# Performance work log

Measured on AMD Instinct MI355X. Metric: run time of the kernel, lower is better.

## Reference

```python
import jax, jax.numpy as jnp
import numpy as np

K_NODES = 4096
SEQ_L = 32
D_MODEL = 128
D_FF = 512
N_EDGES = 65536
LN_EPS = 1e-5
NEG_SLOPE = 0.2  # PyG GATConv default leaky_relu slope


def setup_inputs() -> dict:
    key = jax.random.key(0)
    ks = jax.random.split(key, 12)
    s = 0.02
    D, F = D_MODEL, D_FF
    return {
        "x": jax.random.normal(ks[0], (1, K_NODES, SEQ_L, D), jnp.float32),
        "edge_index": jax.random.randint(ks[1], (1, 2, N_EDGES), 0, K_NODES, dtype=jnp.int64),
        # temporal TransformerEncoderLayer params (norm_first, 1 head, gelu)
        "ln1_g": jnp.ones((D,), jnp.float32), "ln1_b": jnp.zeros((D,), jnp.float32),
        "qkv_w": jax.random.normal(ks[2], (3 * D, D), jnp.float32) * s,
        "qkv_b": jnp.zeros((3 * D,), jnp.float32),
        "out_w": jax.random.normal(ks[3], (D, D), jnp.float32) * s,
        "out_b": jnp.zeros((D,), jnp.float32),
        "ln2_g": jnp.ones((D,), jnp.float32), "ln2_b": jnp.zeros((D,), jnp.float32),
        "ff1_w": jax.random.normal(ks[4], (F, D), jnp.float32) * s,
        "ff1_b": jnp.zeros((F,), jnp.float32),
        "ff2_w": jax.random.normal(ks[5], (D, F), jnp.float32) * s,
        "ff2_b": jnp.zeros((D,), jnp.float32),
        # GATConv params (heads=1, concat -> out dim D)
        "gat_w": jax.random.normal(ks[6], (D, D), jnp.float32) * s,
        "att_src": jax.random.normal(ks[7], (D,), jnp.float32) * s,
        "att_dst": jax.random.normal(ks[8], (D,), jnp.float32) * s,
        "gat_b": jnp.zeros((D,), jnp.float32),
    }


def _ln(x, g, b):
    m = x.mean(-1, keepdims=True)
    v = ((x - m) ** 2).mean(-1, keepdims=True)
    return (x - m) * jax.lax.rsqrt(v + LN_EPS) * g + b


def _temporal(x, ln1_g, ln1_b, qkv_w, qkv_b, out_w, out_b, ln2_g, ln2_b,
              ff1_w, ff1_b, ff2_w, ff2_b):
    # x: [N, L, D]; pre-norm single-head self-attention + GELU FFN
    D = x.shape[-1]
    h = _ln(x, ln1_g, ln1_b)
    qkv = h @ qkv_w.T + qkv_b
    q, k, v = jnp.split(qkv, 3, axis=-1)
    scores = jnp.einsum('nqd,nkd->nqk', q, k) / jnp.sqrt(jnp.asarray(D, x.dtype))
    a = jax.nn.softmax(scores, axis=-1)
    attn = jnp.einsum('nqk,nkd->nqd', a, v) @ out_w.T + out_b
    x = x + attn
    h = _ln(x, ln2_g, ln2_b)
    ff = jax.nn.gelu(h @ ff1_w.T + ff1_b, approximate=False) @ ff2_w.T + ff2_b
    return x + ff


def _gat(x0, src, dst, gat_w, att_src, att_dst, gat_b):
    # x0: [K, L, D]; vectorized over L (replaces the per-timestep python loop)
    K = x0.shape[0]
    h = jnp.einsum('kld,ed->kle', x0, gat_w)              # [K, L, D]
    a_s = jnp.einsum('kld,d->kl', h, att_src)             # [K, L]
    a_d = jnp.einsum('kld,d->kl', h, att_dst)
    e = jax.nn.leaky_relu(a_s[src] + a_d[dst], NEG_SLOPE)  # [E', L]
    m = jax.ops.segment_max(e, dst, num_segments=K)
    ex = jnp.exp(e - m[dst])
    denom = jax.ops.segment_sum(ex, dst, num_segments=K)
    alpha = ex / (denom[dst] + 1e-16)
    out = jax.ops.segment_sum(h[src] * alpha[..., None], dst, num_segments=K)
    return out + gat_b


def reference(x, edge_index, ln1_g, ln1_b, qkv_w, qkv_b, out_w, out_b,
              ln2_g, ln2_b, ff1_w, ff1_b, ff2_w, ff2_b,
              gat_w, att_src, att_dst, gat_b):
    B, K, L, D = x.shape
    xt = _temporal(x.reshape(B * K, L, D), ln1_g, ln1_b, qkv_w, qkv_b,
                   out_w, out_b, ln2_g, ln2_b, ff1_w, ff1_b, ff2_w, ff2_b)
    xt = xt.reshape(B, K, L, D)
    # GATConv adds self-loops by default
    loops = jnp.arange(K, dtype=edge_index.dtype)
    src = jnp.concatenate([edge_index[0, 0], loops])
    dst = jnp.concatenate([edge_index[0, 1], loops])
    out0 = _gat(xt[0], src, dst, gat_w, att_src, att_dst, gat_b)  # [K, L, D]
    res = jnp.zeros_like(x).at[0].set(out0)
    return res
```

## Files before the change

kernel.cpp:

```cpp
#include <hip/hip_runtime.h>

#define KNODES 4096
#define SEQL 32
#define DM 128
#define DFF 512
#define NEDGE 65536
#define NETOT (NEDGE + KNODES)

typedef float f32x4 __attribute__((ext_vector_type(4)));
typedef short s16x8 __attribute__((ext_vector_type(8)));
typedef short s16x4 __attribute__((ext_vector_type(4)));

#define MFMA16(a, b, c) __builtin_amdgcn_mfma_f32_16x16x32_bf16(a, b, c, 0, 0, 0)

#define F_OUT 96
#define F_FF1 128
#define F_FF2 256
#define F_GAT 384
#define NFRAG 416

__device__ __forceinline__ short f2bf(float f) {
  union { float f; unsigned u; } v; v.f = f;
  unsigned r = (v.u + 0x7FFFu + ((v.u >> 16) & 1u)) >> 16;
  return (short)r;
}

__device__ __forceinline__ float gelu_exact(float v) {
  return 0.5f * v * (1.f + erff(v * 0.70710678118654752440f));
}

__device__ __forceinline__ void ln_to_bf16(const float* XF, short* AB,
                                           const float* __restrict__ g,
                                           const float* __restrict__ b,
                                           int r, int cb) {
  const float* xr = XF + r * 132 + cb;
  float v[8]; float s = 0.f, ss = 0.f;
#pragma unroll
  for (int i = 0; i < 8; ++i) { v[i] = xr[i]; s += v[i]; ss += v[i] * v[i]; }
  s += __shfl_xor(s, 1); ss += __shfl_xor(ss, 1);
  s += __shfl_xor(s, 2); ss += __shfl_xor(ss, 2);
  s += __shfl_xor(s, 4); ss += __shfl_xor(ss, 4);
  s += __shfl_xor(s, 8); ss += __shfl_xor(ss, 8);
  const float mean = s * (1.f / 128.f);
  const float var = ss * (1.f / 128.f) - mean * mean;
  const float rs = rsqrtf(var + 1e-5f);
  const float* gp = g + cb; const float* bp = b + cb;
  short o[8];
#pragma unroll
  for (int i = 0; i < 8; ++i) o[i] = f2bf((v[i] - mean) * rs * gp[i] + bp[i]);
  *(s16x8*)(AB + r * 136 + cb) = *(s16x8*)o;
}

__global__ __launch_bounds__(512, 4) void temporal_kernel(
    const float* __restrict__ x,
    const float* __restrict__ ln1_g, const float* __restrict__ ln1_b,
    const short* __restrict__ wpk, const float* __restrict__ qkv_b,
    const float* __restrict__ out_b,
    const float* __restrict__ ln2_g, const float* __restrict__ ln2_b,
    const float* __restrict__ ff1_b, const float* __restrict__ ff2_b,
    const float* __restrict__ att_src, const float* __restrict__ att_dst,
    short* __restrict__ h_out, float* __restrict__ as_out, float* __restrict__ ad_out) {
  __shared__ __align__(16) char smem[53248];
  float* XF = (float*)smem;
  short* AB = (short*)(smem + 16896);
  float* Sf = (float*)(smem + 16896);
  short* Pb = (short*)(smem + 21504);
  short* Qb = (short*)(smem + 25600);
  short* Kb = (short*)(smem + 34304);
  short* Fb = (short*)(smem + 25600);
  short* Vt = (short*)(smem + 43008);

  const int t = threadIdx.x;
  const int w = t >> 6;
  const int lane = t & 63;
  const int q = lane >> 4, c = lane & 15;
  const int n = blockIdx.x;
  const int r16 = t >> 4, cb8 = (t & 15) * 8;

#define WPK(f) ((const s16x8*)(wpk + (size_t)(f) * 512 + lane * 8))

  s16x8 bwq[3][4];
#pragma unroll
  for (int ii = 0; ii < 3; ++ii)
#pragma unroll
    for (int kt = 0; kt < 4; ++kt)
      bwq[ii][kt] = *WPK((w * 3 + ii) * 4 + kt);

  {
#pragma unroll
    for (int i = t; i < 1024; i += 512) {
      const int row = i >> 5, c4i = i & 31;
      *(float4*)(XF + row * 132 + c4i * 4) =
          *(const float4*)(x + (size_t)n * (SEQL * DM) + i * 4);
    }
  }
  __syncthreads();

  ln_to_bf16(XF, AB, ln1_g, ln1_b, r16, cb8);
  __syncthreads();

  {
    s16x8 a[2][4];
#pragma unroll
    for (int mt = 0; mt < 2; ++mt)
#pragma unroll
      for (int kt = 0; kt < 4; ++kt)
        a[mt][kt] = *(const s16x8*)(AB + (mt * 16 + c) * 136 + kt * 32 + q * 8);
#pragma unroll
    for (int ii = 0; ii < 3; ++ii) {
      const int n0 = (w * 3 + ii) * 16;
      f32x4 acc0 = {0.f, 0.f, 0.f, 0.f}, acc1 = {0.f, 0.f, 0.f, 0.f};
#pragma unroll
      for (int kt = 0; kt < 4; ++kt) {
        acc0 = MFMA16(a[0][kt], bwq[ii][kt], acc0);
        acc1 = MFMA16(a[1][kt], bwq[ii][kt], acc1);
      }
      const float bias = qkv_b[n0 + c];
      if (n0 < 128) {
#pragma unroll
        for (int i = 0; i < 4; ++i) {
          Qb[(q * 4 + i) * 136 + n0 + c] = f2bf(acc0[i] + bias);
          Qb[(16 + q * 4 + i) * 136 + n0 + c] = f2bf(acc1[i] + bias);
        }
      } else if (n0 < 256) {
        const int cc = n0 - 128 + c;
#pragma unroll
        for (int i = 0; i < 4; ++i) {
          Kb[(q * 4 + i) * 136 + cc] = f2bf(acc0[i] + bias);
          Kb[(16 + q * 4 + i) * 136 + cc] = f2bf(acc1[i] + bias);
        }
      } else {
        const int d = n0 - 256 + c;
        s16x4 p0, p1;
#pragma unroll
        for (int i = 0; i < 4; ++i) { p0[i] = f2bf(acc0[i] + bias); p1[i] = f2bf(acc1[i] + bias); }
        *(s16x4*)(Vt + d * 40 + q * 4) = p0;
        *(s16x4*)(Vt + d * 40 + 16 + q * 4) = p1;
      }
    }
  }
  __syncthreads();

  if (w < 4) {
    const int mt = w & 1, nt = w >> 1;
    s16x8 aq[4], bk[4];
#pragma unroll
    for (int kt = 0; kt < 4; ++kt) {
      aq[kt] = *(const s16x8*)(Qb + (mt * 16 + c) * 136 + kt * 32 + q * 8);
      bk[kt] = *(const s16x8*)(Kb + (nt * 16 + c) * 136 + kt * 32 + q * 8);
    }
    f32x4 acc = {0.f, 0.f, 0.f, 0.f};
#pragma unroll
    for (int kt = 0; kt < 4; ++kt) acc = MFMA16(aq[kt], bk[kt], acc);
#pragma unroll
    for (int i = 0; i < 4; ++i)
      Sf[(mt * 16 + q * 4 + i) * 36 + nt * 16 + c] = acc[i] * 0.08838834764831845f;
  }
  __syncthreads();

  if (t < 256) {
    const int r8 = t >> 3, c4 = (t & 7) * 4;
    float4 sv = *(const float4*)(Sf + r8 * 36 + c4);
    float mx = fmaxf(fmaxf(sv.x, sv.y), fmaxf(sv.z, sv.w));
    mx = fmaxf(mx, __shfl_xor(mx, 1));
    mx = fmaxf(mx, __shfl_xor(mx, 2));
    mx = fmaxf(mx, __shfl_xor(mx, 4));
    float e0 = expf(sv.x - mx), e1 = expf(sv.y - mx), e2 = expf(sv.z - mx), e3 = expf(sv.w - mx);
    float sum = e0 + e1 + e2 + e3;
    sum += __shfl_xor(sum, 1);
    sum += __shfl_xor(sum, 2);
    sum += __shfl_xor(sum, 4);
    const float inv = 1.f / sum;
    s16x4 pw; pw[0] = f2bf(e0 * inv); pw[1] = f2bf(e1 * inv); pw[2] = f2bf(e2 * inv); pw[3] = f2bf(e3 * inv);
    *(s16x4*)(Pb + r8 * 40 + c4) = pw;
  }
  __syncthreads();

  s16x8 bwp[4];
  {
#pragma unroll
    for (int kt = 0; kt < 4; ++kt) bwp[kt] = *WPK(F_OUT + w * 4 + kt);
    s16x8 ap0 = *(const s16x8*)(Pb + c * 40 + q * 8);
    s16x8 ap1 = *(const s16x8*)(Pb + (16 + c) * 40 + q * 8);
    const int d0 = w * 16;
    s16x8 bv = *(const s16x8*)(Vt + (d0 + c) * 40 + q * 8);
    f32x4 acc0 = {0.f, 0.f, 0.f, 0.f}, acc1 = {0.f, 0.f, 0.f, 0.f};
    acc0 = MFMA16(ap0, bv, acc0);
    acc1 = MFMA16(ap1, bv, acc1);
#pragma unroll
    for (int i = 0; i < 4; ++i) {
      Qb[(q * 4 + i) * 136 + d0 + c] = f2bf(acc0[i]);
      Qb[(16 + q * 4 + i) * 136 + d0 + c] = f2bf(acc1[i]);
    }
  }
  __syncthreads();

  {
    s16x8 aa[2][4];
#pragma unroll
    for (int mt = 0; mt < 2; ++mt)
#pragma unroll
      for (int kt = 0; kt < 4; ++kt)
        aa[mt][kt] = *(const s16x8*)(Qb + (mt * 16 + c) * 136 + kt * 32 + q * 8);
    const int n0 = w * 16;
    f32x4 acc0 = {0.f, 0.f, 0.f, 0.f}, acc1 = {0.f, 0.f, 0.f, 0.f};
#pragma unroll
    for (int kt = 0; kt < 4; ++kt) {
      acc0 = MFMA16(aa[0][kt], bwp[kt], acc0);
      acc1 = MFMA16(aa[1][kt], bwp[kt], acc1);
    }
    const float bias = out_b[n0 + c];
#pragma unroll
    for (int i = 0; i < 4; ++i) {
      XF[(q * 4 + i) * 132 + n0 + c] += acc0[i] + bias;
      XF[(16 + q * 4 + i) * 132 + n0 + c] += acc1[i] + bias;
    }
  }
  __syncthreads();

  ln_to_bf16(XF, AB, ln2_g, ln2_b, r16, cb8);
  __syncthreads();

  {
    s16x8 af[2][4];
#pragma unroll
    for (int mt = 0; mt < 2; ++mt)
#pragma unroll
      for (int kt = 0; kt < 4; ++kt)
        af[mt][kt] = *(const s16x8*)(AB + (mt * 16 + c) * 136 + kt * 32 + q * 8);
    f32x4 facc0 = {0.f, 0.f, 0.f, 0.f}, facc1 = {0.f, 0.f, 0.f, 0.f};

    for (int ch = 0; ch < 2; ++ch) {
      s16x8 bw1[2][4], bw2[8];
#pragma unroll
      for (int ii = 0; ii < 2; ++ii)
#pragma unroll
        for (int kt = 0; kt < 4; ++kt)
          bw1[ii][kt] = *WPK(F_FF1 + (ch * 16 + w * 2 + ii) * 4 + kt);
#pragma unroll
      for (int kt = 0; kt < 8; ++kt)
        bw2[kt] = *WPK(F_FF2 + w * 16 + ch * 8 + kt);

#pragma unroll
      for (int ii = 0; ii < 2; ++ii) {
        const int ntl = w * 2 + ii;
        const int n0g = ch * 256 + ntl * 16;
        f32x4 acc0 = {0.f, 0.f, 0.f, 0.f}, acc1 = {0.f, 0.f, 0.f, 0.f};
#pragma unroll
        for (int kt = 0; kt < 4; ++kt) {
          acc0 = MFMA16(af[0][kt], bw1[ii][kt], acc0);
          acc1 = MFMA16(af[1][kt], bw1[ii][kt], acc1);
        }
        const float bias = ff1_b[n0g + c];
#pragma unroll
        for (int i = 0; i < 4; ++i) {
          Fb[(q * 4 + i) * 264 + ntl * 16 + c] = f2bf(gelu_exact(acc0[i] + bias));
          Fb[(16 + q * 4 + i) * 264 + ntl * 16 + c] = f2bf(gelu_exact(acc1[i] + bias));
        }
      }
      __syncthreads();
#pragma unroll
      for (int kt = 0; kt < 8; ++kt) {
        s16x8 a0 = *(const s16x8*)(Fb + c * 264 + kt * 32 + q * 8);
        s16x8 a1 = *(const s16x8*)(Fb + (16 + c) * 264 + kt * 32 + q * 8);
        facc0 = MFMA16(a0, bw2[kt], facc0);
        facc1 = MFMA16(a1, bw2[kt], facc1);
      }
      __syncthreads();
    }
    {
      const int n0 = w * 16;
      const float bias = ff2_b[n0 + c];
#pragma unroll
      for (int i = 0; i < 4; ++i) {
        const int r0 = q * 4 + i, r1 = 16 + q * 4 + i;
        AB[r0 * 136 + n0 + c] = f2bf(XF[r0 * 132 + n0 + c] + facc0[i] + bias);
        AB[r1 * 136 + n0 + c] = f2bf(XF[r1 * 132 + n0 + c] + facc1[i] + bias);
      }
    }
  }
  s16x8 bwg[4];
#pragma unroll
  for (int kt = 0; kt < 4; ++kt) bwg[kt] = *WPK(F_GAT + w * 4 + kt);
  __syncthreads();

  {
    s16x8 ag[2][4];
#pragma unroll
    for (int mt = 0; mt < 2; ++mt)
#pragma unroll
      for (int kt = 0; kt < 4; ++kt)
        ag[mt][kt] = *(const s16x8*)(AB + (mt * 16 + c) * 136 + kt * 32 + q * 8);
    const int n0 = w * 16;
    f32x4 acc0 = {0.f, 0.f, 0.f, 0.f}, acc1 = {0.f, 0.f, 0.f, 0.f};
#pragma unroll
    for (int kt = 0; kt < 4; ++kt) {
      acc0 = MFMA16(ag[0][kt], bwg[kt], acc0);
      acc1 = MFMA16(ag[1][kt], bwg[kt], acc1);
    }
#pragma unroll
    for (int i = 0; i < 4; ++i) {
      const int r0 = q * 4 + i, r1 = 16 + q * 4 + i;
      XF[r0 * 132 + n0 + c] = acc0[i];
      XF[r1 * 132 + n0 + c] = acc1[i];
    }
  }
  __syncthreads();

  {
    const int row = t >> 4;
    const float* xr = XF + row * 132 + cb8;
    short o[8];
#pragma unroll
    for (int i = 0; i < 8; ++i) o[i] = f2bf(xr[i]);
    *(s16x8*)(h_out + ((size_t)row * KNODES + n) * DM + cb8) = *(s16x8*)o;
  }

  if (t < 64) {
    const int row = t & 31;
    const float* vec = (t < 32) ? att_src : att_dst;
    const float* hr = XF + row * 132;
    float s = 0.f;
#pragma unroll
    for (int d = 0; d < DM; d += 4)
      s += hr[d] * vec[d] + hr[d + 1] * vec[d + 1] + hr[d + 2] * vec[d + 2] + hr[d + 3] * vec[d + 3];
    if (t < 32) as_out[n * SEQL + row] = s;
    else        ad_out[n * SEQL + row] = s;
  }
}

__global__ void cvt_weights(const float* __restrict__ qkv_w, const float* __restrict__ out_w,
                            const float* __restrict__ ff1_w, const float* __restrict__ ff2_w,
                            const float* __restrict__ gat_w, short* __restrict__ wpk) {
  const int u = blockIdx.x * 256 + threadIdx.x;
  if (u >= NFRAG * 64) return;
  const int f = u >> 6, lane = u & 63;
  const int q = lane >> 4, c = lane & 15;
  const float* src; int row, kt, ld;
  if (f < F_OUT)       { src = qkv_w; ld = 128; int g = f;         row = (g >> 2) * 16 + c; kt = g & 3; }
  else if (f < F_FF1)  { src = out_w; ld = 128; int g = f - F_OUT; row = (g >> 2) * 16 + c; kt = g & 3; }
  else if (f < F_FF2)  { src = ff1_w; ld = 128; int g = f - F_FF1; row = (g >> 2) * 16 + c; kt = g & 3; }
  else if (f < F_GAT)  { src = ff2_w; ld = 512; int g = f - F_FF2; row = (g >> 4) * 16 + c; kt = g & 15; }
  else                 { src = gat_w; ld = 128; int g = f - F_GAT; row = (g >> 2) * 16 + c; kt = g & 3; }
  const float* p = src + row * ld + kt * 32 + q * 8;
  const float4 v0 = *(const float4*)p;
  const float4 v1 = *(const float4*)(p + 4);
  s16x8 o;
  o[0] = f2bf(v0.x); o[1] = f2bf(v0.y); o[2] = f2bf(v0.z); o[3] = f2bf(v0.w);
  o[4] = f2bf(v1.x); o[5] = f2bf(v1.y); o[6] = f2bf(v1.z); o[7] = f2bf(v1.w);
  *(s16x8*)(wpk + (size_t)f * 512 + lane * 8) = o;
}

__global__ void zero_counts(int* counts) {
  int i = blockIdx.x * 256 + threadIdx.x;
  if (i < KNODES) counts[i] = 0;
}

__global__ void hist_kernel(const int* __restrict__ ei, int* counts) {
  int i = blockIdx.x * 256 + threadIdx.x;
  if (i < NETOT) {
    int dst = (i < NEDGE) ? ei[NEDGE + i] : (i - NEDGE);
    atomicAdd(&counts[dst], 1);
  }
}

__global__ void scan_kernel(const int* __restrict__ counts, int* offs, int* cursor) {
  __shared__ int tmp[1024];
  const int t = threadIdx.x;
  const int base = t * 4;
  int c0 = counts[base], c1 = counts[base + 1], c2 = counts[base + 2], c3 = counts[base + 3];
  const int s = c0 + c1 + c2 + c3;
  tmp[t] = s;
  __syncthreads();
  for (int off = 1; off < 1024; off <<= 1) {
    int v = (t >= off) ? tmp[t - off] : 0;
    __syncthreads();
    tmp[t] += v;
    __syncthreads();
  }
  int o = tmp[t] - s;
  offs[base] = o; cursor[base] = o; o += c0;
  offs[base + 1] = o; cursor[base + 1] = o; o += c1;
  offs[base + 2] = o; cursor[base + 2] = o; o += c2;
  offs[base + 3] = o; cursor[base + 3] = o; o += c3;
  if (t == 1023) offs[KNODES] = o;
}

__global__ void scatter_kernel(const int* __restrict__ ei, int* cursor, int* __restrict__ csr) {
  int i = blockIdx.x * 256 + threadIdx.x;
  if (i < NETOT) {
    int src, dst;
    if (i < NEDGE) { src = ei[i]; dst = ei[NEDGE + i]; }
    else           { src = dst = i - NEDGE; }
    int pos = atomicAdd(&cursor[dst], 1);
    csr[pos] = src;
  }
}

#define ECH 16
__global__ __launch_bounds__(64) void gat_aggregate(
    const short* __restrict__ h, const float* __restrict__ as_g, const float* __restrict__ ad_g,
    const int* __restrict__ offs, const int* __restrict__ csr,
    const float* __restrict__ gat_b, float* __restrict__ out) {
  __shared__ float ew[ECH * 5];
  __shared__ int   srcs[ECH];

  const int t = threadIdx.x;
  const int lg = blockIdx.x;
  const int n = blockIdx.y;
  const int l0 = lg * 4;

  const int s = t >> 2, lr = t & 3;
  const int r = t >> 4, cl = (t & 15) * 8;

  const float adv = ad_g[n * SEQL + l0 + lr];
  const int beg = offs[n], end = offs[n + 1];
  const size_t rbase = ((size_t)(l0 + r) * KNODES) * DM + cl;

  float dpart = 0.f;
  float acc[8];
#pragma unroll
  for (int j = 0; j < 8; ++j) acc[j] = 0.f;

  for (int cb = beg; cb < end; cb += ECH) {
    const int cnt = min(ECH, end - cb);
    if (s < cnt) {
      const int src = csr[cb + s];
      if (lr == 0) srcs[s] = src;
      float v = as_g[src * SEQL + l0 + lr] + adv;
      v = v > 0.f ? v : 0.2f * v;
      const float e = __expf(v);
      ew[s * 5 + lr] = e;
      dpart += e;
    }
    __syncthreads();

    s16x8 p0, p1, p2, p3;
#define GLOAD(dst, idx)                                                        \
    if ((idx) < cnt)                                                           \
      dst = *(const s16x8*)(h + rbase + (size_t)srcs[idx] * DM)
    GLOAD(p0, 0); GLOAD(p1, 1); GLOAD(p2, 2); GLOAD(p3, 3);

#define CONSUME(p, idx)                                                        \
    if ((idx) < cnt) {                                                         \
      const float wgt = ew[(idx) * 5 + r];                                     \
      const unsigned* pu = (const unsigned*)&(p);                              \
      _Pragma("unroll")                                                        \
      for (int j = 0; j < 4; ++j) {                                           \
        acc[2 * j]     += wgt * __uint_as_float(pu[j] << 16);                  \
        acc[2 * j + 1] += wgt * __uint_as_float(pu[j] & 0xFFFF0000u);          \
      }                                                                        \
    }

    for (int ss = 0; ss < cnt; ss += 4) {
      s16x8 n0, n1, n2, n3;
      GLOAD(n0, ss + 4); GLOAD(n1, ss + 5); GLOAD(n2, ss + 6); GLOAD(n3, ss + 7);
      CONSUME(p0, ss);
      CONSUME(p1, ss + 1);
      CONSUME(p2, ss + 2);
      CONSUME(p3, ss + 3);
      p0 = n0; p1 = n1; p2 = n2; p3 = n3;
    }
#undef GLOAD
#undef CONSUME
    __syncthreads();
  }

  dpart += __shfl_xor(dpart, 4);
  dpart += __shfl_xor(dpart, 8);
  dpart += __shfl_xor(dpart, 16);
  dpart += __shfl_xor(dpart, 32);
  const float iv = 1.f / (__shfl(dpart, r) + 1e-16f);

  const float4 b0 = *(const float4*)(gat_b + cl);
  const float4 b1 = *(const float4*)(gat_b + cl + 4);
  f32x4 o0, o1;
  o0[0] = acc[0] * iv + b0.x; o0[1] = acc[1] * iv + b0.y;
  o0[2] = acc[2] * iv + b0.z; o0[3] = acc[3] * iv + b0.w;
  o1[0] = acc[4] * iv + b1.x; o1[1] = acc[5] * iv + b1.y;
  o1[2] = acc[6] * iv + b1.z; o1[3] = acc[7] * iv + b1.w;
  float* op = out + (size_t)n * (SEQL * DM) + (l0 + r) * DM + cl;
  __builtin_nontemporal_store(o0, (f32x4*)op);
  __builtin_nontemporal_store(o1, (f32x4*)(op + 4));
}

extern "C" void kernel_launch(void* const* d_in, const int* in_sizes, int n_in,
                              void* d_out, int out_size, void* d_ws, size_t ws_size,
                              hipStream_t stream) {
  const float* x       = (const float*)d_in[0];
  const int* ei        = (const int*)d_in[1];
  const float* ln1_g   = (const float*)d_in[2];
  const float* ln1_b   = (const float*)d_in[3];
  const float* qkv_w   = (const float*)d_in[4];
  const float* qkv_b   = (const float*)d_in[5];
  const float* out_w   = (const float*)d_in[6];
  const float* out_b   = (const float*)d_in[7];
  const float* ln2_g   = (const float*)d_in[8];
  const float* ln2_b   = (const float*)d_in[9];
  const float* ff1_w   = (const float*)d_in[10];
  const float* ff1_b   = (const float*)d_in[11];
  const float* ff2_w   = (const float*)d_in[12];
  const float* ff2_b   = (const float*)d_in[13];
  const float* gat_w   = (const float*)d_in[14];
  const float* att_src = (const float*)d_in[15];
  const float* att_dst = (const float*)d_in[16];
  const float* gat_b   = (const float*)d_in[17];
  float* out = (float*)d_out;

  short* h    = (short*)d_ws;
  float* as_g = (float*)(h + (size_t)KNODES * SEQL * DM);
  float* ad_g = as_g + KNODES * SEQL;
  int* counts = (int*)(ad_g + KNODES * SEQL);
  int* offs   = counts + KNODES;
  int* cursor = offs + KNODES + 1;
  int* csr    = cursor + KNODES;
  size_t wofs = (size_t)((char*)(csr + NETOT) - (char*)d_ws);
  wofs = (wofs + 1023) & ~(size_t)1023;
  short* wpk = (short*)((char*)d_ws + wofs);

  cvt_weights<<<(NFRAG * 64 + 255) / 256, 256, 0, stream>>>(qkv_w, out_w, ff1_w, ff2_w, gat_w, wpk);
  zero_counts<<<(KNODES + 255) / 256, 256, 0, stream>>>(counts);
  hist_kernel<<<(NETOT + 255) / 256, 256, 0, stream>>>(ei, counts);
  scan_kernel<<<1, 1024, 0, stream>>>(counts, offs, cursor);
  scatter_kernel<<<(NETOT + 255) / 256, 256, 0, stream>>>(ei, cursor, csr);
  temporal_kernel<<<KNODES, 512, 0, stream>>>(
      x, ln1_g, ln1_b, wpk, qkv_b, out_b, ln2_g, ln2_b,
      ff1_b, ff2_b, att_src, att_dst, h, as_g, ad_g);
  gat_aggregate<<<dim3(8, KNODES), 64, 0, stream>>>(h, as_g, ad_g, offs, csr, gat_b, out);
}
```

Baseline: 330.0 us.

## Pin GAT sequence-group slices to XCDs via persistent atomic work queue

Re-lays out the bf16 node features so each group of 4 sequence positions is contiguous per node. The aggregation kernel becomes a persistent-style kernel. Each block reads its XCC id, takes the sequence group from it, and pulls node indices from a per-group atomic counter. The aim is for each XCD's L2 to hold only its slice of the features (4 MB), so gathers hit L2 instead of crossing dies. It relies on the hardware dispatching blocks evenly across all 8 XCDs. It adds per-node atomics and barriers, and if blocks land unevenly some groups may finish late.

```diff
diff --git a/kernel.cpp b/kernel.cpp
--- a/kernel.cpp
+++ b/kernel.cpp
@@ -313,7 +313,8 @@
     short o[8];
 #pragma unroll
     for (int i = 0; i < 8; ++i) o[i] = f2bf(xr[i]);
-    *(s16x8*)(h_out + ((size_t)row * KNODES + n) * DM + cb8) = *(s16x8*)o;
+    *(s16x8*)(h_out + (((size_t)(row >> 2) * KNODES + n) * 4 + (row & 3)) * DM + cb8) =
+        *(s16x8*)o;
   }
 
   if (t < 64) {
@@ -351,9 +352,10 @@
   *(s16x8*)(wpk + (size_t)f * 512 + lane * 8) = o;
 }
 
-__global__ void zero_counts(int* counts) {
+__global__ void zero_counts(int* counts, int* xcur) {
   int i = blockIdx.x * 256 + threadIdx.x;
   if (i < KNODES) counts[i] = 0;
+  if (i < 8) xcur[i] = 0;
 }
 
 __global__ void hist_kernel(const int* __restrict__ ei, int* counts) {
@@ -398,90 +400,102 @@
 }
 
 #define ECH 16
+#define GAT_BLOCKS 16384
 __global__ __launch_bounds__(64) void gat_aggregate(
     const short* __restrict__ h, const float* __restrict__ as_g, const float* __restrict__ ad_g,
     const int* __restrict__ offs, const int* __restrict__ csr,
-    const float* __restrict__ gat_b, float* __restrict__ out) {
+    const float* __restrict__ gat_b, int* __restrict__ xcur, float* __restrict__ out) {
   __shared__ float ew[ECH * 5];
   __shared__ int   srcs[ECH];
+  __shared__ int   nsh;
 
   const int t = threadIdx.x;
-  const int lg = blockIdx.x;
-  const int n = blockIdx.y;
+  int xcc;
+  asm volatile("s_getreg_b32 %0, hwreg(HW_REG_XCC_ID)" : "=s"(xcc));
+  const int lg = xcc & 7;
   const int l0 = lg * 4;
 
   const int s = t >> 2, lr = t & 3;
   const int r = t >> 4, cl = (t & 15) * 8;
-
-  const float adv = ad_g[n * SEQL + l0 + lr];
-  const int beg = offs[n], end = offs[n + 1];
-  const size_t rbase = ((size_t)(l0 + r) * KNODES) * DM + cl;
-
-  float dpart = 0.f;
-  float acc[8];
-#pragma unroll
-  for (int j = 0; j < 8; ++j) acc[j] = 0.f;
-
-  for (int cb = beg; cb < end; cb += ECH) {
-    const int cnt = min(ECH, end - cb);
-    if (s < cnt) {
-      const int src = csr[cb + s];
-      if (lr == 0) srcs[s] = src;
-      float v = as_g[src * SEQL + l0 + lr] + adv;
-      v = v > 0.f ? v : 0.2f * v;
-      const float e = __expf(v);
-      ew[s * 5 + lr] = e;
-      dpart += e;
-    }
+  const size_t sbase = (size_t)lg * ((size_t)KNODES * 4 * DM) + (size_t)t * 8;
+
+  const float4 b0 = *(const float4*)(gat_b + cl);
+  const float4 b1 = *(const float4*)(gat_b + cl + 4);
+
+  for (;;) {
     __syncthreads();
-
-    s16x8 p0, p1, p2, p3;
+    if (t == 0) nsh = atomicAdd(xcur + lg, 1);
+    __syncthreads();
+    const int n = nsh;
+    if (n >= KNODES) return;
+
+    const float adv = ad_g[n * SEQL + l0 + lr];
+    const int beg = offs[n], end = offs[n + 1];
+
+    float dpart = 0.f;
+    float acc[8];
+#pragma unroll
+    for (int j = 0; j < 8; ++j) acc[j] = 0.f;
+
+    for (int cb = beg; cb < end; cb += ECH) {
+      const int cnt = min(ECH, end - cb);
+      if (s < cnt) {
+        const int src = csr[cb + s];
+        if (lr == 0) srcs[s] = src;
+        float v = as_g[src * SEQL + l0 + lr] + adv;
+        v = v > 0.f ? v : 0.2f * v;
+        const float e = __expf(v);
+        ew[s * 5 + lr] = e;
+        dpart += e;
+      }
+      __syncthreads();
+
+      s16x8 p0, p1, p2, p3;
 #define GLOAD(dst, idx)                                                        \
-    if ((idx) < cnt)                                                           \
-      dst = *(const s16x8*)(h + rbase + (size_t)srcs[idx] * DM)
-    GLOAD(p0, 0); GLOAD(p1, 1); GLOAD(p2, 2); GLOAD(p3, 3);
+      if ((idx) < cnt)                                                         \
+        dst = *(const s16x8*)(h + sbase + (size_t)srcs[idx] * (4 * DM))
+      GLOAD(p0, 0); GLOAD(p1, 1); GLOAD(p2, 2); GLOAD(p3, 3);
 
 #define CONSUME(p, idx)                                                        \
-    if ((idx) < cnt) {                                                         \
-      const float wgt = ew[(idx) * 5 + r];                                     \
-      const unsigned* pu = (const unsigned*)&(p);                              \
-      _Pragma("unroll")                                                        \
-      for (int j = 0; j < 4; ++j) {                                           \
-        acc[2 * j]     += wgt * __uint_as_float(pu[j] << 16);                  \
-        acc[2 * j + 1] += wgt * __uint_as_float(pu[j] & 0xFFFF0000u);          \
-      }                                                                        \
-    }
-
-    for (int ss = 0; ss < cnt; ss += 4) {
-      s16x8 n0, n1, n2, n3;
-      GLOAD(n0, ss + 4); GLOAD(n1, ss + 5); GLOAD(n2, ss + 6); GLOAD(n3, ss + 7);
-      CONSUME(p0, ss);
-      CONSUME(p1, ss + 1);
-      CONSUME(p2, ss + 2);
-      CONSUME(p3, ss + 3);
-      p0 = n0; p1 = n1; p2 = n2; p3 = n3;
-    }
+      if ((idx) < cnt) {                                                       \
+        const float wgt = ew[(idx) * 5 + r];                                   \
+        const unsigned* pu = (const unsigned*)&(p);                            \
+        _Pragma("unroll")                                                      \
+        for (int j = 0; j < 4; ++j) {                                         \
+          acc[2 * j]     += wgt * __uint_as_float(pu[j] << 16);                \
+          acc[2 * j + 1] += wgt * __uint_as_float(pu[j] & 0xFFFF0000u);        \
+        }                                                                      \
+      }
+
+      for (int ss = 0; ss < cnt; ss += 4) {
+        s16x8 n0, n1, n2, n3;
+        GLOAD(n0, ss + 4); GLOAD(n1, ss + 5); GLOAD(n2, ss + 6); GLOAD(n3, ss + 7);
+        CONSUME(p0, ss);
+        CONSUME(p1, ss + 1);
+        CONSUME(p2, ss + 2);
+        CONSUME(p3, ss + 3);
+        p0 = n0; p1 = n1; p2 = n2; p3 = n3;
+      }
 #undef GLOAD
 #undef CONSUME
-    __syncthreads();
-  }
-
-  dpart += __shfl_xor(dpart, 4);
-  dpart += __shfl_xor(dpart, 8);
-  dpart += __shfl_xor(dpart, 16);
-  dpart += __shfl_xor(dpart, 32);
-  const float iv = 1.f / (__shfl(dpart, r) + 1e-16f);
-
-  const float4 b0 = *(const float4*)(gat_b + cl);
-  const float4 b1 = *(const float4*)(gat_b + cl + 4);
-  f32x4 o0, o1;
-  o0[0] = acc[0] * iv + b0.x; o0[1] = acc[1] * iv + b0.y;
-  o0[2] = acc[2] * iv + b0.z; o0[3] = acc[3] * iv + b0.w;
-  o1[0] = acc[4] * iv + b1.x; o1[1] = acc[5] * iv + b1.y;
-  o1[2] = acc[6] * iv + b1.z; o1[3] = acc[7] * iv + b1.w;
-  float* op = out + (size_t)n * (SEQL * DM) + (l0 + r) * DM + cl;
-  __builtin_nontemporal_store(o0, (f32x4*)op);
-  __builtin_nontemporal_store(o1, (f32x4*)(op + 4));
+      __syncthreads();
+    }
+
+    dpart += __shfl_xor(dpart, 4);
+    dpart += __shfl_xor(dpart, 8);
+    dpart += __shfl_xor(dpart, 16);
+    dpart += __shfl_xor(dpart, 32);
+    const float iv = 1.f / (__shfl(dpart, r) + 1e-16f);
+
+    f32x4 o0, o1;
+    o0[0] = acc[0] * iv + b0.x; o0[1] = acc[1] * iv + b0.y;
+    o0[2] = acc[2] * iv + b0.z; o0[3] = acc[3] * iv + b0.w;
+    o1[0] = acc[4] * iv + b1.x; o1[1] = acc[5] * iv + b1.y;
+    o1[2] = acc[6] * iv + b1.z; o1[3] = acc[7] * iv + b1.w;
+    float* op = out + (size_t)n * (SEQL * DM) + (l0 + r) * DM + cl;
+    __builtin_nontemporal_store(o0, (f32x4*)op);
+    __builtin_nontemporal_store(o1, (f32x4*)(op + 4));
+  }
 }
 
 extern "C" void kernel_launch(void* const* d_in, const int* in_sizes, int n_in,
@@ -514,17 +528,18 @@
   int* offs   = counts + KNODES;
   int* cursor = offs + KNODES + 1;
   int* csr    = cursor + KNODES;
-  size_t wofs = (size_t)((char*)(csr + NETOT) - (char*)d_ws);
+  int* xcur   = csr + NETOT;
+  size_t wofs = (size_t)((char*)(xcur + 8) - (char*)d_ws);
   wofs = (wofs + 1023) & ~(size_t)1023;
   short* wpk = (short*)((char*)d_ws + wofs);
 
   cvt_weights<<<(NFRAG * 64 + 255) / 256, 256, 0, stream>>>(qkv_w, out_w, ff1_w, ff2_w, gat_w, wpk);
-  zero_counts<<<(KNODES + 255) / 256, 256, 0, stream>>>(counts);
+  zero_counts<<<(KNODES + 255) / 256, 256, 0, stream>>>(counts, xcur);
   hist_kernel<<<(NETOT + 255) / 256, 256, 0, stream>>>(ei, counts);
   scan_kernel<<<1, 1024, 0, stream>>>(counts, offs, cursor);
   scatter_kernel<<<(NETOT + 255) / 256, 256, 0, stream>>>(ei, cursor, csr);
   temporal_kernel<<<KNODES, 512, 0, stream>>>(
       x, ln1_g, ln1_b, wpk, qkv_b, out_b, ln2_g, ln2_b,
       ff1_b, ff2_b, att_src, att_dst, h, as_g, ad_g);
-  gat_aggregate<<<dim3(8, KNODES), 64, 0, stream>>>(h, as_g, ad_g, offs, csr, gat_b, out);
-}
+  gat_aggregate<<<dim3(GAT_BLOCKS), 64, 0, stream>>>(h, as_g, ad_g, offs, csr, gat_b, xcur, out);
+}
```

New measurement: 857.9 us. +160.0%, slower.
